# Optimization experiments

Measured on AMD Instinct MI355X. Metric: run time of the kernel, lower is better.

## Reference

```python
import jax, jax.numpy as jnp
from jax import lax
import numpy as np

TAU = 1.0          # epoch buffer = 0 -> tau_init * decay^0 = 1.0
NEG = -1.0e9
K_HOP = 2
MAX_CLUSTERS = 16
SIZE_MAX = 8
SIZE_MIN = 1
THRESH = 0.95
EPS = 1e-8


def _gumbel_hard(key, logits, m):
    # torch: logits*mask + (1-mask)*-1e9; gumbel noise; softmax; straight-through one-hot
    mf = m.astype(logits.dtype)
    ml = logits * mf + (1.0 - mf) * NEG
    u = jax.random.uniform(key, logits.shape, dtype=logits.dtype)
    g = -jnp.log(-jnp.log(u + EPS) + EPS)
    soft = jax.nn.softmax((ml + g) / TAU, axis=-1)
    idx = jnp.argmax(soft, axis=-1)
    hard = jax.nn.one_hot(idx, logits.shape[-1], dtype=logits.dtype)
    return hard + soft - lax.stop_gradient(soft), idx


def _k_hop(adj, seed_idx, m):
    # vectorized BFS via masked bmm, fixed K_HOP iterations
    N = adj.shape[1]
    seed = jax.nn.one_hot(seed_idx, N, dtype=bool)
    reach, cur = seed, seed
    for _ in range(K_HOP):
        nb = (jnp.einsum('bn,bnm->bm', cur.astype(adj.dtype), adj) > 0) & m
        new = nb & (~reach)
        reach = reach | nb
        cur = new
    return reach


def _topk_gumbel(key, logits, k, m):
    # iterative hard gumbel selection of up to k nodes per batch (k: [B] int)
    sel = jnp.zeros_like(logits)
    remaining = m
    for step in range(SIZE_MAX - SIZE_MIN):
        key, sk = jax.random.split(key)
        active = (step < k) & remaining.any(-1)
        step_mask = remaining & active[:, None]
        s, _ = _gumbel_hard(sk, logits, step_mask)
        sel = sel + s * active[:, None].astype(sel.dtype)
        remaining = remaining & ~(lax.stop_gradient(s) > 0.5)
    return sel


def _gru_seq(hist, h0, Wih, Whh, bih, bhh):
    # torch nn.GRU cell math, scan over time; hist [B,T,D], h0 [B,H]
    H = h0.shape[-1]
    def step(h, xt):
        gi = xt @ Wih.T + bih
        gh = h @ Whh.T + bhh
        r = jax.nn.sigmoid(gi[:, :H] + gh[:, :H])
        z = jax.nn.sigmoid(gi[:, H:2 * H] + gh[:, H:2 * H])
        n = jnp.tanh(gi[:, 2 * H:] + r * gh[:, 2 * H:])
        return (1.0 - z) * n + z * h, None
    h_final, _ = lax.scan(step, h0, jnp.swapaxes(hist, 0, 1))
    return h_final


def _forward(x, adj, mask, sel_w1, sel_b1, sel_w2, sel_b2,
             size_w1, size_b1, size_w2, size_b2,
             gru_wih, gru_whh, gru_bih, gru_bhh, init_w, init_b):
    B, N, D = x.shape
    H = init_w.shape[0]
    maskf = mask.astype(x.dtype)
    total = maskf.sum(-1)                                   # [B]
    x_mean = (x * maskf[:, :, None]).sum(1) / (total[:, None] + EPS)
    ctx_hidden = x_mean @ init_w.T + init_b                 # [B,H]
    global_ctx = ctx_hidden
    assignment = jnp.zeros((B, N, MAX_CLUSTERS), x.dtype)
    assigned = jnp.zeros((B, N), bool)
    history = []
    key = jax.random.key(42)
    size_range = jnp.arange(SIZE_MAX - SIZE_MIN + 1)
    for c in range(MAX_CLUSTERS):
        # gradient-safe early termination: mask contributions instead of breaking
        pct = assignment.sum((1, 2)) / (total + EPS)
        active = (pct < THRESH) & (total > 0)
        avail = mask & (~assigned)
        # selection MLP on [x, context]
        sel_in = jnp.concatenate(
            [x, jnp.broadcast_to(global_ctx[:, None, :], (B, N, H))], -1)
        h1 = jax.nn.relu(sel_in @ sel_w1.T + sel_b1)
        logits = (h1 @ sel_w2.T + sel_b2)[..., 0]           # [B,N]
        key, k1, k2, k3 = jax.random.split(key, 4)
        seed_sel, seed_idx = _gumbel_hard(k1, logits, avail)
        seed_feat = jnp.einsum('bn,bnd->bd', seed_sel, x)
        khop = _k_hop(adj, seed_idx, avail)
        candidates = khop & avail
        max_possible = jnp.minimum(candidates.sum(-1), SIZE_MAX)
        # cluster-size prediction
        size_in = jnp.concatenate(
            [seed_feat, global_ctx, max_possible.astype(x.dtype)[:, None]], -1)
        sh = jax.nn.relu(size_in @ size_w1.T + size_b1)
        size_logits = sh @ size_w2.T + size_b2              # [B,8]
        valid_ranges = jnp.clip(max_possible - SIZE_MIN + 1, 1, size_logits.shape[-1])
        range_mask = size_range[None, :] < valid_ranges[:, None]
        size_sel, _ = _gumbel_hard(k2, size_logits, range_mask)
        sizes = jnp.argmax(size_sel, -1) + SIZE_MIN         # [B]
        seed_oh = jax.nn.one_hot(seed_idx, N, dtype=bool)
        extra = _topk_gumbel(k3, logits, sizes - 1, candidates & (~seed_oh))
        cluster_sel = (seed_sel + extra) * active.astype(x.dtype)[:, None]
        assignment = assignment.at[:, :, c].set(cluster_sel)
        assigned = assigned | (lax.stop_gradient(cluster_sel) > 0.5)
        # gradient-safe cluster embedding (mean over selected nodes)
        csize = jnp.maximum(lax.stop_gradient(cluster_sel).sum(-1), 1.0)
        emb = jnp.einsum('bn,bnd->bd', cluster_sel, x) / csize[:, None]
        emb = emb * active.astype(x.dtype)[:, None]
        history.append(emb)
        # update_context_safe: rerun GRU on full history from current hidden
        hist = jnp.stack(history, 1)                        # [B,t+1,D]
        ctx_hidden = _gru_seq(hist, ctx_hidden, gru_wih, gru_whh, gru_bih, gru_bhh)
        global_ctx = ctx_hidden
    return assignment


def setup_inputs() -> dict:
    key = jax.random.key(0)
    ks = jax.random.split(key, 16)
    B, N, D, H = 32, 512, 128, 128
    x = jax.random.normal(ks[0], (B, N, D), jnp.float32)
    a = (jax.random.uniform(ks[1], (B, N, N)) < 0.02).astype(jnp.float32)
    adj = jnp.maximum(a, jnp.swapaxes(a, 1, 2))             # symmetric binary contacts
    mask = jnp.ones((B, N), bool)
    s = 0.05
    p = lambda k, sh: jax.random.normal(k, sh, jnp.float32) * s
    return dict(
        x=x, adj=adj, mask=mask,
        sel_w1=p(ks[2], (H, D + H)), sel_b1=p(ks[3], (H,)),
        sel_w2=p(ks[4], (1, H)), sel_b2=p(ks[5], (1,)),
        size_w1=p(ks[6], (H, D + H + 1)), size_b1=p(ks[7], (H,)),
        size_w2=p(ks[8], (SIZE_MAX, H)), size_b2=p(ks[9], (SIZE_MAX,)),
        gru_wih=p(ks[10], (3 * H, D)), gru_whh=p(ks[11], (3 * H, H)),
        gru_bih=p(ks[12], (3 * H,)), gru_bhh=p(ks[13], (3 * H,)),
        init_w=p(ks[14], (H, D)), init_b=p(ks[15], (H,)))


def reference(x, adj, mask, sel_w1, sel_b1, sel_w2, sel_b2,
              size_w1, size_b1, size_w2, size_b2,
              gru_wih, gru_whh, gru_bih, gru_bhh, init_w, init_b):
    return _forward(x, adj, mask, sel_w1, sel_b1, sel_w2, sel_b2,
                    size_w1, size_b1, size_w2, size_b2,
                    gru_wih, gru_whh, gru_bih, gru_bhh, init_w, init_b)
```

## Files before the change

### kernel.cpp

```cpp
#include <hip/hip_runtime.h>
#include <stdint.h>


#define NBATCH 32
#define NNODE  512
#define NDIM   128
#define NHID   128
#define NCLUS  16
#define NEGV   (-1.0e9f)
#define EPSF   (1e-8f)

struct KeyPack {
  uint32_t k1[NCLUS][2];
  uint32_t k2[NCLUS][2];
  uint32_t sk[NCLUS][7][2];
};

__host__ __device__ inline void tf2x32(uint32_t k0, uint32_t k1,
                                       uint32_t x0, uint32_t x1,
                                       uint32_t& o0, uint32_t& o1) {
  uint32_t k2 = k0 ^ k1 ^ 0x1BD11BDAu;
#define TFR(r) { x0 += x1; x1 = (x1 << (r)) | (x1 >> (32 - (r))); x1 ^= x0; }
  x0 += k0; x1 += k1;
  TFR(13) TFR(15) TFR(26) TFR(6)
  x0 += k1; x1 += k2 + 1u;
  TFR(17) TFR(29) TFR(16) TFR(24)
  x0 += k2; x1 += k0 + 2u;
  TFR(13) TFR(15) TFR(26) TFR(6)
  x0 += k0; x1 += k1 + 3u;
  TFR(17) TFR(29) TFR(16) TFR(24)
  x0 += k1; x1 += k2 + 4u;
  TFR(13) TFR(15) TFR(26) TFR(6)
  x0 += k2; x1 += k0 + 5u;
#undef TFR
  o0 = x0; o1 = x1;
}

__device__ __forceinline__ float jax_uniform(uint32_t k0, uint32_t k1, uint32_t j) {
  uint32_t a, b;
  tf2x32(k0, k1, 0u, j, a, b);
  uint32_t bits = a ^ b;
  return __uint_as_float((bits >> 9) | 0x3F800000u) - 1.0f;
}

__device__ __forceinline__ float gumb(float u) {
  return -logf(-logf(u + EPSF) + EPSF);
}

__device__ __forceinline__ float sigmf(float v) { return 1.0f / (1.0f + expf(-v)); }


__global__ void k_transpose(const float* __restrict__ gwih,
                            const float* __restrict__ gwhh,
                            const float* __restrict__ selw1, const float* __restrict__ szw1,
                            const float* __restrict__ initw,
                            float4* __restrict__ Wi3, float4* __restrict__ W3,
                            float* __restrict__ W1cT, float* __restrict__ szW1T,
                            float* __restrict__ initWT) {
  int t = blockIdx.x * blockDim.x + threadIdx.x;
  if (t < 32 * 384) {
    int i = t % 384, j4 = t / 384;
    const float* si = gwih + i * 128 + j4 * 4;
    Wi3[t] = make_float4(si[0], si[1], si[2], si[3]);
    const float* sh = gwhh + i * 128 + j4 * 4;
    W3[t]  = make_float4(sh[0], sh[1], sh[2], sh[3]);
  }
  if (t < 128 * 128) {
    int j = t >> 7, hh = t & 127;
    W1cT[t]   = selw1[hh * 256 + 128 + j];
    initWT[t] = initw[hh * 128 + j];
  }
  if (t < 257 * 128) {
    int j = t >> 7, i = t & 127;
    szW1T[t] = szw1[i * 257 + j];
  }
}

__global__ void k_adjbits(const float* __restrict__ adj, uint8_t* __restrict__ adjb8) {
  int t = blockIdx.x * blockDim.x + threadIdx.x;
  if (t >= NBATCH * NNODE * 64) return;
  const float4* p = (const float4*)adj + (size_t)t * 2;
  float4 a = p[0], b = p[1];
  uint32_t m = (a.x > 0.f ? 1u : 0u) | (a.y > 0.f ? 2u : 0u)
             | (a.z > 0.f ? 4u : 0u) | (a.w > 0.f ? 8u : 0u)
             | (b.x > 0.f ? 16u : 0u) | (b.y > 0.f ? 32u : 0u)
             | (b.z > 0.f ? 64u : 0u) | (b.w > 0.f ? 128u : 0u);
  adjb8[t] = (uint8_t)m;
}

__global__ __launch_bounds__(512)
void k_xw1(const float* __restrict__ x, const float* __restrict__ selw1,
           float* __restrict__ xw1T) {
  const int b = blockIdx.x >> 3;
  const int n0 = (blockIdx.x & 7) * 64;
  __shared__ float xs[64][NDIM + 1];
  for (int i = threadIdx.x; i < 64 * NDIM; i += 512) {
    int n = i >> 7, d = i & 127;
    xs[n][d] = x[((size_t)b * NNODE + n0 + n) * NDIM + d];
  }
  __syncthreads();
  for (int p = threadIdx.x; p < 64 * NHID; p += 512) {
    int h = p >> 6, n = p & 63;
    const float* wr = selw1 + h * 256;
    float a0 = 0.f, a1 = 0.f, a2 = 0.f, a3 = 0.f;
#pragma unroll 8
    for (int d = 0; d < NDIM; d += 4) {
      a0 = fmaf(xs[n][d + 0], wr[d + 0], a0);
      a1 = fmaf(xs[n][d + 1], wr[d + 1], a1);
      a2 = fmaf(xs[n][d + 2], wr[d + 2], a2);
      a3 = fmaf(xs[n][d + 3], wr[d + 3], a3);
    }
    xw1T[((size_t)b * NHID + h) * NNODE + n0 + n] = (a0 + a1) + (a2 + a3);
  }
}


#define MV384_PARTIALS(WP4, V4, PART)                                        \
  {                                                                          \
    const float4 cv0 = (V4)[wid * 4 + 0], cv1 = (V4)[wid * 4 + 1];           \
    const float4 cv2 = (V4)[wid * 4 + 2], cv3 = (V4)[wid * 4 + 3];           \
    _Pragma("unroll")                                                        \
    for (int m = 0; m < 6; m++) {                                            \
      const int row = lane + 64 * m;                                         \
      float4 w0 = (WP4)[row], w1 = (WP4)[384 + row];                         \
      float4 w2 = (WP4)[768 + row], w3v = (WP4)[1152 + row];                 \
      float pa = w0.x * cv0.x, pb = w0.y * cv0.y;                            \
      pa = fmaf(w0.z, cv0.z, pa);  pb = fmaf(w0.w, cv0.w, pb);               \
      pa = fmaf(w1.x, cv1.x, pa);  pb = fmaf(w1.y, cv1.y, pb);               \
      pa = fmaf(w1.z, cv1.z, pa);  pb = fmaf(w1.w, cv1.w, pb);               \
      pa = fmaf(w2.x, cv2.x, pa);  pb = fmaf(w2.y, cv2.y, pb);               \
      pa = fmaf(w2.z, cv2.z, pa);  pb = fmaf(w2.w, cv2.w, pb);               \
      pa = fmaf(w3v.x, cv3.x, pa); pb = fmaf(w3v.y, cv3.y, pb);              \
      pa = fmaf(w3v.z, cv3.z, pa); pb = fmaf(w3v.w, cv3.w, pb);              \
      (PART)[wid * 384 + row] = pa + pb;                                     \
    }                                                                        \
  }

__global__ __launch_bounds__(512)
void k_main(const float* __restrict__ x,
            const float* __restrict__ selb1, const float* __restrict__ selw2,
            const float* __restrict__ selb2,
            const float* __restrict__ szb1, const float* __restrict__ szw2,
            const float* __restrict__ szb2,
            const float* __restrict__ gbih, const float* __restrict__ gbhh,
            const float* __restrict__ initb,
            const float* __restrict__ xw1T, const uint32_t* __restrict__ adjb,
            const float4* __restrict__ Wi3, const float4* __restrict__ W3,
            const float* __restrict__ W1cT, const float* __restrict__ szW1T,
            const float* __restrict__ initWT,
            float* __restrict__ out, KeyPack kp)
{
  const int b = blockIdx.x;
  const int t = threadIdx.x;
  const int lane = t & 63, wid = t >> 6;

  __shared__ __align__(16) float4 resW[6144];
  __shared__ __align__(16) float gic[NCLUS][3 * NHID];
  __shared__ __align__(16) float partf[6144];
  __shared__ __align__(16) float gbhh_s[384];
  __shared__ __align__(16) float ctxb[NHID];
  __shared__ __align__(16) float ctxterm[NHID];
  __shared__ __align__(16) float cat256[2 * NHID];
  __shared__ __align__(16) float embs[NDIM];
  __shared__ __align__(16) float h1s[NHID];
  __shared__ __align__(16) float xm[NHID];
  __shared__ __align__(16) float selw2s[NHID];
  __shared__ float slog[8];
  __shared__ int   ibox[4];
  __shared__ uint32_t availw[16];
  __shared__ uint32_t curm[16];
  __shared__ uint32_t selm[16];

#pragma unroll
  for (int i = 0; i < 12; i++) {
    int idx = i * 512 + t;
    int dch = idx / 384, row = idx % 384;
    int sj4 = 4 * (dch >> 1) + (dch & 1);
    resW[idx] = W3[(size_t)sj4 * 384 + row];
  }
  if (t < 384) gbhh_s[t] = gbhh[t];
  if (t < NHID) selw2s[t] = selw2[t];
  const float selb2_r = selb2[0];
  const float szb2_r  = szb2[wid];
  const float selb1_r = (t < NHID) ? selb1[t] : 0.f;
  const float szb1_r  = (t < NHID) ? szb1[t] : 0.f;
  const float szw1mp_r = (t < NHID) ? szW1T[256 * NHID + t] : 0.f;
  const float gbih_r  = (t < 384) ? gbih[t] : 0.f;

  {
    const int j = t & 127, p = t >> 7;
    const float* xp = x + ((size_t)b * NNODE + p * 128) * NDIM + j;
    float a0 = 0.f, a1 = 0.f, a2 = 0.f, a3 = 0.f;
#pragma unroll 4
    for (int n = 0; n < 128; n += 4) {
      a0 += xp[(size_t)(n + 0) * NDIM];
      a1 += xp[(size_t)(n + 1) * NDIM];
      a2 += xp[(size_t)(n + 2) * NDIM];
      a3 += xp[(size_t)(n + 3) * NDIM];
    }
    partf[p * 128 + j] = (a0 + a1) + (a2 + a3);
  }
  __syncthreads();
  if (t < NHID) xm[t] = (partf[t] + partf[128 + t] + partf[256 + t] + partf[384 + t]) * (1.0f / 512.0f);
  __syncthreads();
  if (t < NHID) {
    float a = initb[t];
    const float4* x4 = (const float4*)xm;
#pragma unroll 8
    for (int j4 = 0; j4 < 32; j4++) {
      float4 v = x4[j4];
      int j = 4 * j4;
      a = fmaf(v.x, initWT[(j + 0) * NHID + t], a);
      a = fmaf(v.y, initWT[(j + 1) * NHID + t], a);
      a = fmaf(v.z, initWT[(j + 2) * NHID + t], a);
      a = fmaf(v.w, initWT[(j + 3) * NHID + t], a);
    }
    ctxb[t] = a;
  }
  __syncthreads();

  bool assigned = false;
  uint32_t selbits = 0u;

  for (int c = 0; c < NCLUS; c++) {
    {
      const int hh = t & 127, p = t >> 7;
      const float4* c4 = (const float4*)(ctxb + p * 32);
      float a0 = 0.f, a1 = 0.f, a2 = 0.f, a3 = 0.f;
#pragma unroll
      for (int j4 = 0; j4 < 8; j4++) {
        float4 cv = c4[j4];
        int j = p * 32 + j4 * 4;
        a0 = fmaf(cv.x, W1cT[(j + 0) * NHID + hh], a0);
        a1 = fmaf(cv.y, W1cT[(j + 1) * NHID + hh], a1);
        a2 = fmaf(cv.z, W1cT[(j + 2) * NHID + hh], a2);
        a3 = fmaf(cv.w, W1cT[(j + 3) * NHID + hh], a3);
      }
      partf[p * 128 + hh] = (a0 + a1) + (a2 + a3);
    }
    __syncthreads();
    if (t < NHID) ctxterm[t] = selb1_r + partf[t] + partf[128 + t] + partf[256 + t] + partf[384 + t];
    __syncthreads();

    float myLogit;
    {
      float acc0 = selb2_r, acc1 = 0.f, acc2 = 0.f, acc3 = 0.f;
      const float* xp = xw1T + (size_t)b * NHID * NNODE + t;
      const float4* ct4 = (const float4*)ctxterm;
      const float4* w24 = (const float4*)selw2s;
#pragma unroll 8
      for (int h4 = 0; h4 < 32; h4++) {
        float4 cv = ct4[h4], wv = w24[h4];
        int h = h4 * 4;
        acc0 = fmaf(fmaxf(xp[(size_t)(h + 0) * NNODE] + cv.x, 0.f), wv.x, acc0);
        acc1 = fmaf(fmaxf(xp[(size_t)(h + 1) * NNODE] + cv.y, 0.f), wv.y, acc1);
        acc2 = fmaf(fmaxf(xp[(size_t)(h + 2) * NNODE] + cv.z, 0.f), wv.z, acc2);
        acc3 = fmaf(fmaxf(xp[(size_t)(h + 3) * NNODE] + cv.w, 0.f), wv.w, acc3);
      }
      myLogit = (acc0 + acc1) + (acc2 + acc3);
    }
    {
      const bool avail = !assigned;
      float z = (avail ? myLogit : NEGV)
              + gumb(jax_uniform(kp.k1[c][0], kp.k1[c][1], (uint32_t)(b * NNODE + t)));
      partf[t] = z;
      partf[4096 + t] = myLogit;
#pragma unroll
      for (int s = 0; s < 7; s++)
        partf[512 + s * 512 + t] =
            gumb(jax_uniform(kp.sk[c][s][0], kp.sk[c][s][1], (uint32_t)(b * NNODE + t)));
      unsigned long long ab = __ballot(!assigned);
      if (lane == 0) { availw[2 * wid] = (uint32_t)ab; availw[2 * wid + 1] = (uint32_t)(ab >> 32); }
    }
    __syncthreads();

    if (wid == 0) {
      float bv = -3.4e38f; int bi = 0x7fffffff;
#pragma unroll
      for (int k = 0; k < 8; k++) {
        float v = partf[lane + 64 * k];
        if (v > bv) { bv = v; bi = lane + 64 * k; }
      }
#pragma unroll
      for (int off = 32; off > 0; off >>= 1) {
        float ov = __shfl_down(bv, off); int oi = __shfl_down(bi, off);
        if (ov > bv || (ov == bv && oi < bi)) { bv = ov; bi = oi; }
      }
      const int seed = __shfl(bi, 0);
      const float cf0 = x[((size_t)b * NNODE + seed) * NDIM + lane];
      const float cf1 = x[((size_t)b * NNODE + seed) * NDIM + 64 + lane];

      uint32_t av[16], reach[16], cw[16];
#pragma unroll
      for (int k = 0; k < 16; k++) av[k] = availw[k];
#pragma unroll
      for (int k = 0; k < 16; k++) {
        uint32_t s0 = ((seed >> 5) == k) ? (1u << (seed & 31)) : 0u;
        reach[k] = s0; cw[k] = s0;
      }
#pragma unroll
      for (int hop = 0; hop < 2; hop++) {
        uint32_t carrier = 0u;
#pragma unroll
        for (int k = 0; k < 16; k++) carrier = (lane == k) ? cw[k] : carrier;
        uint32_t myw = __shfl(carrier, lane >> 2);
        uint32_t mybyte = (myw >> ((lane & 3) * 8)) & 0xffu;
        uint32_t acc[16];
#pragma unroll
        for (int k = 0; k < 16; k++) acc[k] = 0u;
        while (mybyte) {
          int b2 = __ffs(mybyte) - 1; mybyte &= mybyte - 1;
          const uint4* r4 = (const uint4*)(adjb + ((size_t)b * NNODE + 8 * lane + b2) * 16);
          uint4 q0 = r4[0], q1 = r4[1], q2 = r4[2], q3 = r4[3];
          acc[0] |= q0.x; acc[1] |= q0.y; acc[2]  |= q0.z; acc[3]  |= q0.w;
          acc[4] |= q1.x; acc[5] |= q1.y; acc[6]  |= q1.z; acc[7]  |= q1.w;
          acc[8] |= q2.x; acc[9] |= q2.y; acc[10] |= q2.z; acc[11] |= q2.w;
          acc[12] |= q3.x; acc[13] |= q3.y; acc[14] |= q3.z; acc[15] |= q3.w;
        }
#pragma unroll
        for (int off = 1; off < 64; off <<= 1) {
#pragma unroll
          for (int k = 0; k < 16; k++) acc[k] |= __shfl_xor(acc[k], off);
        }
#pragma unroll
        for (int k = 0; k < 16; k++) {
          uint32_t nb = acc[k] & av[k];
          uint32_t nw = nb & ~reach[k];
          reach[k] |= nb;
          cw[k] = nw;
        }
      }
      int cnt = 0;
#pragma unroll
      for (int k = 0; k < 16; k++) cnt += __popc(reach[k]);
      if (lane == 0) {
        ibox[0] = seed; ibox[1] = min(cnt, 8); ibox[3] = cnt;
#pragma unroll
        for (int k = 0; k < 16; k++) curm[k] = reach[k];
      }
      cat256[lane] = cf0;
      cat256[64 + lane] = cf1;
    } else if (wid == 1) {
      cat256[NHID + lane] = ctxb[lane];
      cat256[NHID + 64 + lane] = ctxb[64 + lane];
    }
    __syncthreads();
    const int mp = ibox[1];

    {
      const int hh = t & 127, p = t >> 7;
      const float4* c4 = (const float4*)(cat256 + p * 64);
      float a0 = 0.f, a1 = 0.f, a2 = 0.f, a3 = 0.f;
#pragma unroll
      for (int j4 = 0; j4 < 16; j4++) {
        float4 cv = c4[j4];
        int j = p * 64 + j4 * 4;
        a0 = fmaf(cv.x, szW1T[(j + 0) * NHID + hh], a0);
        a1 = fmaf(cv.y, szW1T[(j + 1) * NHID + hh], a1);
        a2 = fmaf(cv.z, szW1T[(j + 2) * NHID + hh], a2);
        a3 = fmaf(cv.w, szW1T[(j + 3) * NHID + hh], a3);
      }
      partf[p * 128 + hh] = (a0 + a1) + (a2 + a3);
    }
    __syncthreads();
    if (t < NHID) {
      float a = szb1_r + ((partf[t] + partf[128 + t]) + (partf[256 + t] + partf[384 + t]))
              + (float)mp * szw1mp_r;
      h1s[t] = fmaxf(a, 0.f);
    }
    __syncthreads();
    {
      float a = h1s[lane] * szw2[wid * NHID + lane]
              + h1s[64 + lane] * szw2[wid * NHID + 64 + lane];
#pragma unroll
      for (int off = 32; off > 0; off >>= 1) a += __shfl_down(a, off);
      if (lane == 0) {
        float g2 = gumb(jax_uniform(kp.k2[c][0], kp.k2[c][1], (uint32_t)(b * 8 + wid)));
        slog[wid] = ((wid < mp) ? (a + szb2_r) : NEGV) + g2;
      }
    }
    __syncthreads();

    if (wid == 0) {
      float bv0 = slog[0]; int kextra = 0;
#pragma unroll
      for (int q = 1; q < 8; q++) if (slog[q] > bv0) { bv0 = slog[q]; kextra = q; }
      const int seed = ibox[0];
      uint32_t sw[16], remw[16];
#pragma unroll
      for (int k = 0; k < 16; k++) {
        uint32_t cwv = curm[k];
        uint32_t sb = ((seed >> 5) == k) ? (1u << (seed & 31)) : 0u;
        sw[k] = sb;
        remw[k] = cwv & ~sb;
      }
      int remcnt = ibox[3] - 1;
      int selcnt = 1;
      for (int s = 0; s < kextra; s++) {
        if (remcnt <= 0) break;
        uint32_t carrier = 0u;
#pragma unroll
        for (int k = 0; k < 16; k++) carrier = (lane == k) ? remw[k] : carrier;
        uint32_t myw = __shfl(carrier, lane >> 2);
        uint32_t mybyte = (myw >> ((lane & 3) * 8)) & 0xffu;
        float bv = -3.4e38f; int bi = 0x7fffffff;
#pragma unroll
        for (int b2 = 0; b2 < 8; b2++) {
          int n = 8 * lane + b2;
          float g  = partf[512 + s * 512 + n];
          float lg = partf[4096 + n];
          float v = ((mybyte >> b2) & 1u) ? (lg + g) : (NEGV + g);
          if (v > bv) { bv = v; bi = n; }
        }
#pragma unroll
        for (int off = 32; off > 0; off >>= 1) {
          float ov = __shfl_down(bv, off); int oi = __shfl_down(bi, off);
          if (ov > bv || (ov == bv && oi < bi)) { bv = ov; bi = oi; }
        }
        const int pick = __shfl(bi, 0);
#pragma unroll
        for (int k = 0; k < 16; k++) {
          uint32_t bit = ((pick >> 5) == k) ? (1u << (pick & 31)) : 0u;
          sw[k] |= bit;
          remw[k] &= ~bit;
        }
        remcnt--; selcnt++;
      }
      if (lane == 0) {
#pragma unroll
        for (int k = 0; k < 16; k++) selm[k] = sw[k];
        ibox[2] = selcnt;
      }
    }
    __syncthreads();

    {
      const bool sel = ((selm[t >> 5] >> (t & 31)) & 1u) != 0u;
      if (sel) selbits |= (1u << c);
      assigned = assigned || sel;
    }
    if (t < NDIM) {
      float a = 0.f;
      for (int w = 0; w < 16; w++) {
        uint32_t mwd = selm[w];
        while (mwd) {
          int bit = __ffs(mwd) - 1;
          mwd &= mwd - 1;
          a += x[((size_t)b * NNODE + (w * 32 + bit)) * NDIM + t];
        }
      }
      embs[t] = a / (float)ibox[2];
    }
    __syncthreads();

    {
      uintptr_t wp = (uintptr_t)Wi3;
      asm volatile("" : "+s"(wp));
      const float4* wi = (const float4*)wp + (size_t)wid * 4 * 384;
      const float4* e4 = (const float4*)embs;
      MV384_PARTIALS(wi, e4, partf)
    }
    __syncthreads();
    if (t < 384) {
      gic[c][t] = gbih_r
                + (((partf[t] + partf[384 + t]) + (partf[768 + t] + partf[1152 + t]))
                 + ((partf[1536 + t] + partf[1920 + t]) + (partf[2304 + t] + partf[2688 + t])));
    }
    __syncthreads();

    {
      const float4* cb4 = (const float4*)ctxb;
      float4 cv0 = cb4[wid * 4 + 0], cv1 = cb4[wid * 4 + 1];
      float4 cv2 = cb4[wid * 4 + 2], cv3 = cb4[wid * 4 + 3];
      for (int tt = 0; tt <= c; tt++) {
        float* pdst = partf + ((tt & 1) ? 3072 : 0);
        {
          uintptr_t gwp = (uintptr_t)W3;
          asm volatile("" : "+s"(gwp));
          const float4* ws = (const float4*)gwp;
#pragma unroll
          for (int m = 0; m < 6; m++) {
            const int row = lane + 64 * m;
            float4 w0 = resW[(2 * wid + 0) * 384 + row];
            float4 w1 = resW[(2 * wid + 1) * 384 + row];
            float4 w2 = ws[(size_t)(4 * wid + 2) * 384 + row];
            float4 w3v = ws[(size_t)(4 * wid + 3) * 384 + row];
            float pa = w0.x * cv0.x, pb = w0.y * cv0.y;
            pa = fmaf(w0.z, cv0.z, pa);  pb = fmaf(w0.w, cv0.w, pb);
            pa = fmaf(w1.x, cv1.x, pa);  pb = fmaf(w1.y, cv1.y, pb);
            pa = fmaf(w1.z, cv1.z, pa);  pb = fmaf(w1.w, cv1.w, pb);
            pa = fmaf(w2.x, cv2.x, pa);  pb = fmaf(w2.y, cv2.y, pb);
            pa = fmaf(w2.z, cv2.z, pa);  pb = fmaf(w2.w, cv2.w, pb);
            pa = fmaf(w3v.x, cv3.x, pa); pb = fmaf(w3v.y, cv3.y, pb);
            pa = fmaf(w3v.z, cv3.z, pa); pb = fmaf(w3v.w, cv3.w, pb);
            pdst[wid * 384 + row] = pa + pb;
          }
        }
        __syncthreads();
        float nv = 0.f;
        if (lane < 16) {
          const int u = 16 * wid + lane;
          const float* pp = partf + ((tt & 1) ? 3072 : 0);
          float ghr = ((pp[u]        + pp[384 + u])  + (pp[768 + u]  + pp[1152 + u]))
                    + ((pp[1536 + u] + pp[1920 + u]) + (pp[2304 + u] + pp[2688 + u]));
          float ghz = ((pp[128 + u]  + pp[512 + u])  + (pp[896 + u]  + pp[1280 + u]))
                    + ((pp[1664 + u] + pp[2048 + u]) + (pp[2432 + u] + pp[2816 + u]));
          float ghn = ((pp[256 + u]  + pp[640 + u])  + (pp[1024 + u] + pp[1408 + u]))
                    + ((pp[1792 + u] + pp[2176 + u]) + (pp[2560 + u] + pp[2944 + u]));
          const float* gi = gic[tt];
          float r  = sigmf(gi[u] + ghr + gbhh_s[u]);
          float zz = sigmf(gi[NHID + u] + ghz + gbhh_s[NHID + u]);
          float nn = tanhf(gi[2 * NHID + u] + r * (ghn + gbhh_s[2 * NHID + u]));
          float4 cc = (lane & 8) ? ((lane & 4) ? cv3 : cv2) : ((lane & 4) ? cv1 : cv0);
          float old = (lane & 2) ? ((lane & 1) ? cc.w : cc.z) : ((lane & 1) ? cc.y : cc.x);
          nv = (1.f - zz) * nn + zz * old;
        }
        if (tt == c) {
          if (lane < 16) ctxb[16 * wid + lane] = nv;
        } else {
          cv0 = make_float4(__shfl(nv, 0),  __shfl(nv, 1),  __shfl(nv, 2),  __shfl(nv, 3));
          cv1 = make_float4(__shfl(nv, 4),  __shfl(nv, 5),  __shfl(nv, 6),  __shfl(nv, 7));
          cv2 = make_float4(__shfl(nv, 8),  __shfl(nv, 9),  __shfl(nv, 10), __shfl(nv, 11));
          cv3 = make_float4(__shfl(nv, 12), __shfl(nv, 13), __shfl(nv, 14), __shfl(nv, 15));
        }
      }
    }
    __syncthreads();
  }

  float4* o4 = (float4*)(out + ((size_t)b * NNODE + t) * NCLUS);
#pragma unroll
  for (int q = 0; q < 4; q++) {
    float4 v;
    v.x = (selbits >> (4 * q + 0)) & 1u ? 1.f : 0.f;
    v.y = (selbits >> (4 * q + 1)) & 1u ? 1.f : 0.f;
    v.z = (selbits >> (4 * q + 2)) & 1u ? 1.f : 0.f;
    v.w = (selbits >> (4 * q + 3)) & 1u ? 1.f : 0.f;
    o4[q] = v;
  }
}


extern "C" void kernel_launch(void* const* d_in, const int* in_sizes, int n_in,
                              void* d_out, int out_size, void* d_ws, size_t ws_size,
                              hipStream_t stream) {
  (void)in_sizes; (void)n_in; (void)out_size; (void)ws_size;

  const float* x     = (const float*)d_in[0];
  const float* adj   = (const float*)d_in[1];
  const float* selw1 = (const float*)d_in[3];
  const float* selb1 = (const float*)d_in[4];
  const float* selw2 = (const float*)d_in[5];
  const float* selb2 = (const float*)d_in[6];
  const float* szw1  = (const float*)d_in[7];
  const float* szb1  = (const float*)d_in[8];
  const float* szw2  = (const float*)d_in[9];
  const float* szb2  = (const float*)d_in[10];
  const float* gwih  = (const float*)d_in[11];
  const float* gwhh  = (const float*)d_in[12];
  const float* gbih  = (const float*)d_in[13];
  const float* gbhh  = (const float*)d_in[14];
  const float* initw = (const float*)d_in[15];
  const float* initb = (const float*)d_in[16];
  float* out = (float*)d_out;

  float*    xw1T   = (float*)d_ws;
  uint32_t* adjb   = (uint32_t*)(xw1T + (size_t)NBATCH * NHID * NNODE);
  float*    Wi3    = (float*)(adjb + (size_t)NBATCH * NNODE * 16);
  float*    W3     = Wi3 + 384 * 128;
  float*    W1cT   = W3 + 384 * 128;
  float*    szW1T  = W1cT + 128 * 128;
  float*    initWT = szW1T + 257 * 128;

  KeyPack kp;
  uint32_t kk0 = 0u, kk1 = 42u;
  for (int c = 0; c < NCLUS; c++) {
    uint32_t nk0, nk1, t0, t1, u0, u1;
    tf2x32(kk0, kk1, 0u, 0u, nk0, nk1);
    tf2x32(kk0, kk1, 0u, 1u, kp.k1[c][0], kp.k1[c][1]);
    tf2x32(kk0, kk1, 0u, 2u, kp.k2[c][0], kp.k2[c][1]);
    tf2x32(kk0, kk1, 0u, 3u, t0, t1);
    for (int s = 0; s < 7; s++) {
      tf2x32(t0, t1, 0u, 1u, kp.sk[c][s][0], kp.sk[c][s][1]);
      tf2x32(t0, t1, 0u, 0u, u0, u1);
      t0 = u0; t1 = u1;
    }
    kk0 = nk0; kk1 = nk1;
  }

  k_transpose<<<192, 256, 0, stream>>>(gwih, gwhh, selw1, szw1, initw,
                                       (float4*)Wi3, (float4*)W3,
                                       W1cT, szW1T, initWT);
  k_adjbits<<<(NBATCH * NNODE * 64) / 256, 256, 0, stream>>>(adj, (uint8_t*)adjb);
  k_xw1<<<NBATCH * 8, 512, 0, stream>>>(x, selw1, xw1T);
  k_main<<<NBATCH, 512, 0, stream>>>(x, selb1, selw2, selb2, szb1, szw2, szb2,
                                     gbih, gbhh, initb, xw1T, adjb,
                                     (const float4*)Wi3, (const float4*)W3,
                                     W1cT, szW1T, initWT, out, kp);
}
```

Baseline: 816.7 us.

## Double k_main block to 1024 threads and keep GRU weights in registers

The main per-batch kernel now runs 1024 threads instead of 512, so each wave handles half as many weight columns in the GRU recurrences and MLP reductions. The recurrent weights are loaded once per cluster into registers instead of being staged in a large shared-memory copy plus streamed from global. Gumbel noise generation moves to the upper 512 threads so it runs alongside the logit computation. In exchange there are more partials to reduce, reduction and GRU update are serialized onto 128 threads with an extra barrier per recurrent step, and register pressure under a 1024-thread launch bound may cause spills.

```diff
diff --git a/kernel.cpp b/kernel.cpp
--- a/kernel.cpp
+++ b/kernel.cpp
@@ -115,28 +115,7 @@
 }
 
 
-#define MV384_PARTIALS(WP4, V4, PART)                                        \
-  {                                                                          \
-    const float4 cv0 = (V4)[wid * 4 + 0], cv1 = (V4)[wid * 4 + 1];           \
-    const float4 cv2 = (V4)[wid * 4 + 2], cv3 = (V4)[wid * 4 + 3];           \
-    _Pragma("unroll")                                                        \
-    for (int m = 0; m < 6; m++) {                                            \
-      const int row = lane + 64 * m;                                         \
-      float4 w0 = (WP4)[row], w1 = (WP4)[384 + row];                         \
-      float4 w2 = (WP4)[768 + row], w3v = (WP4)[1152 + row];                 \
-      float pa = w0.x * cv0.x, pb = w0.y * cv0.y;                            \
-      pa = fmaf(w0.z, cv0.z, pa);  pb = fmaf(w0.w, cv0.w, pb);               \
-      pa = fmaf(w1.x, cv1.x, pa);  pb = fmaf(w1.y, cv1.y, pb);               \
-      pa = fmaf(w1.z, cv1.z, pa);  pb = fmaf(w1.w, cv1.w, pb);               \
-      pa = fmaf(w2.x, cv2.x, pa);  pb = fmaf(w2.y, cv2.y, pb);               \
-      pa = fmaf(w2.z, cv2.z, pa);  pb = fmaf(w2.w, cv2.w, pb);               \
-      pa = fmaf(w3v.x, cv3.x, pa); pb = fmaf(w3v.y, cv3.y, pb);              \
-      pa = fmaf(w3v.z, cv3.z, pa); pb = fmaf(w3v.w, cv3.w, pb);              \
-      (PART)[wid * 384 + row] = pa + pb;                                     \
-    }                                                                        \
-  }
-
-__global__ __launch_bounds__(512)
+__global__ __launch_bounds__(1024)
 void k_main(const float* __restrict__ x,
             const float* __restrict__ selb1, const float* __restrict__ selw2,
             const float* __restrict__ selb2,
@@ -154,10 +133,10 @@
   const int t = threadIdx.x;
   const int lane = t & 63, wid = t >> 6;
 
-  __shared__ __align__(16) float4 resW[6144];
+  __shared__ __align__(16) float part[16 * 384];
+  __shared__ __align__(16) float selbuf[9 * 512];
+  __shared__ __align__(16) float mlppart[8 * 128];
   __shared__ __align__(16) float gic[NCLUS][3 * NHID];
-  __shared__ __align__(16) float partf[6144];
-  __shared__ __align__(16) float gbhh_s[384];
   __shared__ __align__(16) float ctxb[NHID];
   __shared__ __align__(16) float ctxterm[NHID];
   __shared__ __align__(16) float cat256[2 * NHID];
@@ -171,37 +150,36 @@
   __shared__ uint32_t curm[16];
   __shared__ uint32_t selm[16];
 
-#pragma unroll
-  for (int i = 0; i < 12; i++) {
-    int idx = i * 512 + t;
-    int dch = idx / 384, row = idx % 384;
-    int sj4 = 4 * (dch >> 1) + (dch & 1);
-    resW[idx] = W3[(size_t)sj4 * 384 + row];
-  }
-  if (t < 384) gbhh_s[t] = gbhh[t];
   if (t < NHID) selw2s[t] = selw2[t];
   const float selb2_r = selb2[0];
-  const float szb2_r  = szb2[wid];
+  const float szb2_r  = (wid < 8) ? szb2[wid] : 0.f;
   const float selb1_r = (t < NHID) ? selb1[t] : 0.f;
   const float szb1_r  = (t < NHID) ? szb1[t] : 0.f;
   const float szw1mp_r = (t < NHID) ? szW1T[256 * NHID + t] : 0.f;
   const float gbih_r  = (t < 384) ? gbih[t] : 0.f;
+  float gb0 = 0.f, gb1 = 0.f, gb2 = 0.f;
+  if (t < NHID) { gb0 = gbhh[t]; gb1 = gbhh[NHID + t]; gb2 = gbhh[2 * NHID + t]; }
 
   {
     const int j = t & 127, p = t >> 7;
-    const float* xp = x + ((size_t)b * NNODE + p * 128) * NDIM + j;
+    const float* xp = x + ((size_t)b * NNODE + p * 64) * NDIM + j;
     float a0 = 0.f, a1 = 0.f, a2 = 0.f, a3 = 0.f;
 #pragma unroll 4
-    for (int n = 0; n < 128; n += 4) {
+    for (int n = 0; n < 64; n += 4) {
       a0 += xp[(size_t)(n + 0) * NDIM];
       a1 += xp[(size_t)(n + 1) * NDIM];
       a2 += xp[(size_t)(n + 2) * NDIM];
       a3 += xp[(size_t)(n + 3) * NDIM];
     }
-    partf[p * 128 + j] = (a0 + a1) + (a2 + a3);
+    part[p * 128 + j] = (a0 + a1) + (a2 + a3);
   }
   __syncthreads();
-  if (t < NHID) xm[t] = (partf[t] + partf[128 + t] + partf[256 + t] + partf[384 + t]) * (1.0f / 512.0f);
+  if (t < NHID) {
+    float s = 0.f;
+#pragma unroll
+    for (int p = 0; p < 8; p++) s += part[p * 128 + t];
+    xm[t] = s * (1.0f / 512.0f);
+  }
   __syncthreads();
   if (t < NHID) {
     float a = initb[t];
@@ -225,25 +203,29 @@
   for (int c = 0; c < NCLUS; c++) {
     {
       const int hh = t & 127, p = t >> 7;
-      const float4* c4 = (const float4*)(ctxb + p * 32);
+      const float4* c4 = (const float4*)(ctxb + p * 16);
       float a0 = 0.f, a1 = 0.f, a2 = 0.f, a3 = 0.f;
 #pragma unroll
-      for (int j4 = 0; j4 < 8; j4++) {
+      for (int j4 = 0; j4 < 4; j4++) {
         float4 cv = c4[j4];
-        int j = p * 32 + j4 * 4;
+        int j = p * 16 + j4 * 4;
         a0 = fmaf(cv.x, W1cT[(j + 0) * NHID + hh], a0);
         a1 = fmaf(cv.y, W1cT[(j + 1) * NHID + hh], a1);
         a2 = fmaf(cv.z, W1cT[(j + 2) * NHID + hh], a2);
         a3 = fmaf(cv.w, W1cT[(j + 3) * NHID + hh], a3);
       }
-      partf[p * 128 + hh] = (a0 + a1) + (a2 + a3);
-    }
-    __syncthreads();
-    if (t < NHID) ctxterm[t] = selb1_r + partf[t] + partf[128 + t] + partf[256 + t] + partf[384 + t];
-    __syncthreads();
-
-    float myLogit;
-    {
+      mlppart[p * 128 + hh] = (a0 + a1) + (a2 + a3);
+    }
+    __syncthreads();
+    if (t < NHID) {
+      float s = selb1_r;
+#pragma unroll
+      for (int p = 0; p < 8; p++) s += mlppart[p * 128 + t];
+      ctxterm[t] = s;
+    }
+    __syncthreads();
+
+    if (t < 512) {
       float acc0 = selb2_r, acc1 = 0.f, acc2 = 0.f, acc3 = 0.f;
       const float* xp = xw1T + (size_t)b * NHID * NNODE + t;
       const float4* ct4 = (const float4*)ctxterm;
@@ -257,20 +239,16 @@
         acc2 = fmaf(fmaxf(xp[(size_t)(h + 2) * NNODE] + cv.z, 0.f), wv.z, acc2);
         acc3 = fmaf(fmaxf(xp[(size_t)(h + 3) * NNODE] + cv.w, 0.f), wv.w, acc3);
       }
-      myLogit = (acc0 + acc1) + (acc2 + acc3);
-    }
-    {
-      const bool avail = !assigned;
-      float z = (avail ? myLogit : NEGV)
-              + gumb(jax_uniform(kp.k1[c][0], kp.k1[c][1], (uint32_t)(b * NNODE + t)));
-      partf[t] = z;
-      partf[4096 + t] = myLogit;
-#pragma unroll
-      for (int s = 0; s < 7; s++)
-        partf[512 + s * 512 + t] =
-            gumb(jax_uniform(kp.sk[c][s][0], kp.sk[c][s][1], (uint32_t)(b * NNODE + t)));
+      selbuf[t] = (acc0 + acc1) + (acc2 + acc3);
       unsigned long long ab = __ballot(!assigned);
       if (lane == 0) { availw[2 * wid] = (uint32_t)ab; availw[2 * wid + 1] = (uint32_t)(ab >> 32); }
+    } else {
+      const uint32_t n = (uint32_t)(t - 512);
+      selbuf[512 + n] = gumb(jax_uniform(kp.k1[c][0], kp.k1[c][1], (uint32_t)b * NNODE + n));
+#pragma unroll
+      for (int s = 0; s < 7; s++)
+        selbuf[1024 + s * 512 + n] =
+            gumb(jax_uniform(kp.sk[c][s][0], kp.sk[c][s][1], (uint32_t)b * NNODE + n));
     }
     __syncthreads();
 
@@ -278,8 +256,10 @@
       float bv = -3.4e38f; int bi = 0x7fffffff;
 #pragma unroll
       for (int k = 0; k < 8; k++) {
-        float v = partf[lane + 64 * k];
-        if (v > bv) { bv = v; bi = lane + 64 * k; }
+        int n = lane + 64 * k;
+        bool av = (availw[n >> 5] >> (n & 31)) & 1u;
+        float v = (av ? selbuf[n] : NEGV) + selbuf[512 + n];
+        if (v > bv) { bv = v; bi = n; }
       }
 #pragma unroll
       for (int off = 32; off > 0; off >>= 1) {
@@ -349,27 +329,28 @@
 
     {
       const int hh = t & 127, p = t >> 7;
-      const float4* c4 = (const float4*)(cat256 + p * 64);
+      const float4* c4 = (const float4*)(cat256 + p * 32);
       float a0 = 0.f, a1 = 0.f, a2 = 0.f, a3 = 0.f;
 #pragma unroll
-      for (int j4 = 0; j4 < 16; j4++) {
+      for (int j4 = 0; j4 < 8; j4++) {
         float4 cv = c4[j4];
-        int j = p * 64 + j4 * 4;
+        int j = p * 32 + j4 * 4;
         a0 = fmaf(cv.x, szW1T[(j + 0) * NHID + hh], a0);
         a1 = fmaf(cv.y, szW1T[(j + 1) * NHID + hh], a1);
         a2 = fmaf(cv.z, szW1T[(j + 2) * NHID + hh], a2);
         a3 = fmaf(cv.w, szW1T[(j + 3) * NHID + hh], a3);
       }
-      partf[p * 128 + hh] = (a0 + a1) + (a2 + a3);
+      mlppart[p * 128 + hh] = (a0 + a1) + (a2 + a3);
     }
     __syncthreads();
     if (t < NHID) {
-      float a = szb1_r + ((partf[t] + partf[128 + t]) + (partf[256 + t] + partf[384 + t]))
-              + (float)mp * szw1mp_r;
-      h1s[t] = fmaxf(a, 0.f);
-    }
-    __syncthreads();
-    {
+      float s = szb1_r + (float)mp * szw1mp_r;
+#pragma unroll
+      for (int p = 0; p < 8; p++) s += mlppart[p * 128 + t];
+      h1s[t] = fmaxf(s, 0.f);
+    }
+    __syncthreads();
+    if (wid < 8) {
       float a = h1s[lane] * szw2[wid * NHID + lane]
               + h1s[64 + lane] * szw2[wid * NHID + 64 + lane];
 #pragma unroll
@@ -407,8 +388,8 @@
 #pragma unroll
         for (int b2 = 0; b2 < 8; b2++) {
           int n = 8 * lane + b2;
-          float g  = partf[512 + s * 512 + n];
-          float lg = partf[4096 + n];
+          float g  = selbuf[1024 + s * 512 + n];
+          float lg = selbuf[n];
           float v = ((mybyte >> b2) & 1u) ? (lg + g) : (NEGV + g);
           if (v > bv) { bv = v; bi = n; }
         }
@@ -434,7 +415,7 @@
     }
     __syncthreads();
 
-    {
+    if (t < 512) {
       const bool sel = ((selm[t >> 5] >> (t & 31)) & 1u) != 0u;
       if (sel) selbits |= (1u << c);
       assigned = assigned || sel;
@@ -456,87 +437,86 @@
     {
       uintptr_t wp = (uintptr_t)Wi3;
       asm volatile("" : "+s"(wp));
-      const float4* wi = (const float4*)wp + (size_t)wid * 4 * 384;
-      const float4* e4 = (const float4*)embs;
-      MV384_PARTIALS(wi, e4, partf)
+      const float4* wi = (const float4*)wp;
+      const float4 ev0 = ((const float4*)embs)[wid * 2 + 0];
+      const float4 ev1 = ((const float4*)embs)[wid * 2 + 1];
+#pragma unroll
+      for (int m = 0; m < 6; m++) {
+        const int row = lane + 64 * m;
+        float4 w0 = wi[(size_t)(2 * wid + 0) * 384 + row];
+        float4 w1 = wi[(size_t)(2 * wid + 1) * 384 + row];
+        float pa = w0.x * ev0.x, pb = w0.y * ev0.y;
+        pa = fmaf(w0.z, ev0.z, pa); pb = fmaf(w0.w, ev0.w, pb);
+        pa = fmaf(w1.x, ev1.x, pa); pb = fmaf(w1.y, ev1.y, pb);
+        pa = fmaf(w1.z, ev1.z, pa); pb = fmaf(w1.w, ev1.w, pb);
+        part[wid * 384 + row] = pa + pb;
+      }
     }
     __syncthreads();
     if (t < 384) {
-      gic[c][t] = gbih_r
-                + (((partf[t] + partf[384 + t]) + (partf[768 + t] + partf[1152 + t]))
-                 + ((partf[1536 + t] + partf[1920 + t]) + (partf[2304 + t] + partf[2688 + t])));
+      float s = gbih_r;
+#pragma unroll
+      for (int w = 0; w < 16; w++) s += part[w * 384 + t];
+      gic[c][t] = s;
     }
     __syncthreads();
 
     {
-      const float4* cb4 = (const float4*)ctxb;
-      float4 cv0 = cb4[wid * 4 + 0], cv1 = cb4[wid * 4 + 1];
-      float4 cv2 = cb4[wid * 4 + 2], cv3 = cb4[wid * 4 + 3];
+      uintptr_t gwp = (uintptr_t)W3;
+      asm volatile("" : "+s"(gwp));
+      const float4* ws = (const float4*)gwp;
+      float4 wreg[12];
+#pragma unroll
+      for (int m = 0; m < 6; m++) {
+        wreg[2 * m + 0] = ws[(size_t)(2 * wid + 0) * 384 + lane + 64 * m];
+        wreg[2 * m + 1] = ws[(size_t)(2 * wid + 1) * 384 + lane + 64 * m];
+      }
       for (int tt = 0; tt <= c; tt++) {
-        float* pdst = partf + ((tt & 1) ? 3072 : 0);
         {
-          uintptr_t gwp = (uintptr_t)W3;
-          asm volatile("" : "+s"(gwp));
-          const float4* ws = (const float4*)gwp;
+          const float4 cv0 = ((const float4*)ctxb)[wid * 2 + 0];
+          const float4 cv1 = ((const float4*)ctxb)[wid * 2 + 1];
 #pragma unroll
           for (int m = 0; m < 6; m++) {
             const int row = lane + 64 * m;
-            float4 w0 = resW[(2 * wid + 0) * 384 + row];
-            float4 w1 = resW[(2 * wid + 1) * 384 + row];
-            float4 w2 = ws[(size_t)(4 * wid + 2) * 384 + row];
-            float4 w3v = ws[(size_t)(4 * wid + 3) * 384 + row];
-            float pa = w0.x * cv0.x, pb = w0.y * cv0.y;
-            pa = fmaf(w0.z, cv0.z, pa);  pb = fmaf(w0.w, cv0.w, pb);
-            pa = fmaf(w1.x, cv1.x, pa);  pb = fmaf(w1.y, cv1.y, pb);
-            pa = fmaf(w1.z, cv1.z, pa);  pb = fmaf(w1.w, cv1.w, pb);
-            pa = fmaf(w2.x, cv2.x, pa);  pb = fmaf(w2.y, cv2.y, pb);
-            pa = fmaf(w2.z, cv2.z, pa);  pb = fmaf(w2.w, cv2.w, pb);
-            pa = fmaf(w3v.x, cv3.x, pa); pb = fmaf(w3v.y, cv3.y, pb);
-            pa = fmaf(w3v.z, cv3.z, pa); pb = fmaf(w3v.w, cv3.w, pb);
-            pdst[wid * 384 + row] = pa + pb;
+            float4 wa = wreg[2 * m], wb = wreg[2 * m + 1];
+            float pa = wa.x * cv0.x, pb = wa.y * cv0.y;
+            pa = fmaf(wa.z, cv0.z, pa); pb = fmaf(wa.w, cv0.w, pb);
+            pa = fmaf(wb.x, cv1.x, pa); pb = fmaf(wb.y, cv1.y, pb);
+            pa = fmaf(wb.z, cv1.z, pa); pb = fmaf(wb.w, cv1.w, pb);
+            part[wid * 384 + row] = pa + pb;
           }
         }
         __syncthreads();
-        float nv = 0.f;
-        if (lane < 16) {
-          const int u = 16 * wid + lane;
-          const float* pp = partf + ((tt & 1) ? 3072 : 0);
-          float ghr = ((pp[u]        + pp[384 + u])  + (pp[768 + u]  + pp[1152 + u]))
-                    + ((pp[1536 + u] + pp[1920 + u]) + (pp[2304 + u] + pp[2688 + u]));
-          float ghz = ((pp[128 + u]  + pp[512 + u])  + (pp[896 + u]  + pp[1280 + u]))
-                    + ((pp[1664 + u] + pp[2048 + u]) + (pp[2432 + u] + pp[2816 + u]));
-          float ghn = ((pp[256 + u]  + pp[640 + u])  + (pp[1024 + u] + pp[1408 + u]))
-                    + ((pp[1792 + u] + pp[2176 + u]) + (pp[2560 + u] + pp[2944 + u]));
+        if (t < NHID) {
+          float ghr = 0.f, ghz = 0.f, ghn = 0.f;
+#pragma unroll
+          for (int w = 0; w < 16; w++) {
+            ghr += part[w * 384 + t];
+            ghz += part[w * 384 + 128 + t];
+            ghn += part[w * 384 + 256 + t];
+          }
           const float* gi = gic[tt];
-          float r  = sigmf(gi[u] + ghr + gbhh_s[u]);
-          float zz = sigmf(gi[NHID + u] + ghz + gbhh_s[NHID + u]);
-          float nn = tanhf(gi[2 * NHID + u] + r * (ghn + gbhh_s[2 * NHID + u]));
-          float4 cc = (lane & 8) ? ((lane & 4) ? cv3 : cv2) : ((lane & 4) ? cv1 : cv0);
-          float old = (lane & 2) ? ((lane & 1) ? cc.w : cc.z) : ((lane & 1) ? cc.y : cc.x);
-          nv = (1.f - zz) * nn + zz * old;
-        }
-        if (tt == c) {
-          if (lane < 16) ctxb[16 * wid + lane] = nv;
-        } else {
-          cv0 = make_float4(__shfl(nv, 0),  __shfl(nv, 1),  __shfl(nv, 2),  __shfl(nv, 3));
-          cv1 = make_float4(__shfl(nv, 4),  __shfl(nv, 5),  __shfl(nv, 6),  __shfl(nv, 7));
-          cv2 = make_float4(__shfl(nv, 8),  __shfl(nv, 9),  __shfl(nv, 10), __shfl(nv, 11));
-          cv3 = make_float4(__shfl(nv, 12), __shfl(nv, 13), __shfl(nv, 14), __shfl(nv, 15));
-        }
-      }
-    }
-    __syncthreads();
-  }
-
-  float4* o4 = (float4*)(out + ((size_t)b * NNODE + t) * NCLUS);
-#pragma unroll
-  for (int q = 0; q < 4; q++) {
-    float4 v;
-    v.x = (selbits >> (4 * q + 0)) & 1u ? 1.f : 0.f;
-    v.y = (selbits >> (4 * q + 1)) & 1u ? 1.f : 0.f;
-    v.z = (selbits >> (4 * q + 2)) & 1u ? 1.f : 0.f;
-    v.w = (selbits >> (4 * q + 3)) & 1u ? 1.f : 0.f;
-    o4[q] = v;
+          float r  = sigmf(gi[t] + ghr + gb0);
+          float zz = sigmf(gi[NHID + t] + ghz + gb1);
+          float nn = tanhf(gi[2 * NHID + t] + r * (ghn + gb2));
+          ctxb[t] = (1.f - zz) * nn + zz * ctxb[t];
+        }
+        __syncthreads();
+      }
+    }
+  }
+
+  if (t < 512) {
+    float4* o4 = (float4*)(out + ((size_t)b * NNODE + t) * NCLUS);
+#pragma unroll
+    for (int q = 0; q < 4; q++) {
+      float4 v;
+      v.x = (selbits >> (4 * q + 0)) & 1u ? 1.f : 0.f;
+      v.y = (selbits >> (4 * q + 1)) & 1u ? 1.f : 0.f;
+      v.z = (selbits >> (4 * q + 2)) & 1u ? 1.f : 0.f;
+      v.w = (selbits >> (4 * q + 3)) & 1u ? 1.f : 0.f;
+      o4[q] = v;
+    }
   }
 }
 
@@ -593,8 +573,8 @@
                                        W1cT, szW1T, initWT);
   k_adjbits<<<(NBATCH * NNODE * 64) / 256, 256, 0, stream>>>(adj, (uint8_t*)adjb);
   k_xw1<<<NBATCH * 8, 512, 0, stream>>>(x, selw1, xw1T);
-  k_main<<<NBATCH, 512, 0, stream>>>(x, selb1, selw2, selb2, szb1, szw2, szb2,
-                                     gbih, gbhh, initb, xw1T, adjb,
-                                     (const float4*)Wi3, (const float4*)W3,
-                                     W1cT, szW1T, initWT, out, kp);
-}
+  k_main<<<NBATCH, 1024, 0, stream>>>(x, selb1, selw2, selb2, szb1, szw2, szb2,
+                                      gbih, gbhh, initb, xw1T, adjb,
+                                      (const float4*)Wi3, (const float4*)W3,
+                                      W1cT, szW1T, initWT, out, kp);
+}
```

Result: no change. 811.9 us (-0.6%).
